# Optimization experiments

Measured on AMD Instinct MI355X. Metric: run time of the kernel, lower is better.

The kernel has to match this reference:

```python
import jax, jax.numpy as jnp
import numpy as np

S, B, I, H, L, O = 2048, 64, 64, 128, 2, 1


def _lstm_dir(xs, w_ih, w_hh, b, reverse):
    # xs: (S, B, in); w_ih: (4H, in); w_hh: (4H, H); b: (4H,) = b_ih + b_hh
    # PyTorch gate order: i, f, g, o
    gx = jnp.einsum('sbi,gi->sbg', xs, w_ih) + b  # precompute input gates once
    h0 = jnp.zeros((xs.shape[1], w_hh.shape[1]), xs.dtype)
    c0 = jnp.zeros_like(h0)

    def step(carry, g_t):
        h, c = carry
        g = g_t + h @ w_hh.T
        i, f, gg, o = jnp.split(g, 4, axis=-1)
        i = jax.nn.sigmoid(i)
        f = jax.nn.sigmoid(f)
        gg = jnp.tanh(gg)
        o = jax.nn.sigmoid(o)
        c = f * c + i * gg
        h = o * jnp.tanh(c)
        return (h, c), h

    _, hs = jax.lax.scan(step, (h0, c0), gx, reverse=reverse)
    return hs  # (S, B, H), time-aligned for both directions (PyTorch semantics)


def _bilstm(x, layers):
    out = x
    for (wif, whf, bf, wir, whr, br) in layers:
        hf = _lstm_dir(out, wif, whf, bf, reverse=False)
        hb = _lstm_dir(out, wir, whr, br, reverse=True)
        out = jnp.concatenate([hf, hb], axis=-1)  # (S, B, 2H)
    return out


def setup_inputs() -> dict:
    key = jax.random.key(0)
    ks = jax.random.split(key, 16)
    sc = 1.0 / np.sqrt(H)
    u = lambda k, shp: jax.random.uniform(k, shp, jnp.float32, -sc, sc)
    inp = {
        'x': jax.random.normal(ks[0], (S, B, I), jnp.float32),
        # layer 0 (input size I)
        'w_ih_f0': u(ks[1], (4 * H, I)), 'w_hh_f0': u(ks[2], (4 * H, H)), 'b_f0': u(ks[3], (4 * H,)),
        'w_ih_r0': u(ks[4], (4 * H, I)), 'w_hh_r0': u(ks[5], (4 * H, H)), 'b_r0': u(ks[6], (4 * H,)),
        # layer 1 (input size 2H)
        'w_ih_f1': u(ks[7], (4 * H, 2 * H)), 'w_hh_f1': u(ks[8], (4 * H, H)), 'b_f1': u(ks[9], (4 * H,)),
        'w_ih_r1': u(ks[10], (4 * H, 2 * H)), 'w_hh_r1': u(ks[11], (4 * H, H)), 'b_r1': u(ks[12], (4 * H,)),
        # final linear: (O, 2H), (O,)
        'w_out': u(ks[13], (O, 2 * H)), 'b_out': u(ks[14], (O,)),
    }
    return inp


def reference(x, w_ih_f0, w_hh_f0, b_f0, w_ih_r0, w_hh_r0, b_r0,
              w_ih_f1, w_hh_f1, b_f1, w_ih_r1, w_hh_r1, b_r1, w_out, b_out):
    layers = [
        (w_ih_f0, w_hh_f0, b_f0, w_ih_r0, w_hh_r0, b_r0),
        (w_ih_f1, w_hh_f1, b_f1, w_ih_r1, w_hh_r1, b_r1),
    ]
    h = _bilstm(x, layers)                      # (S, B, 2H)
    y = jnp.einsum('sbh,oh->sbo', h, w_out) + b_out  # linear over flattened (s*b, h)
    return y
```

## Files before the change

kernel.cpp:

```cpp
#include <hip/hip_runtime.h>
#include <hip/hip_bf16.h>

#define SEQ 2048
#define NB  64

typedef _Float16 f16x8 __attribute__((ext_vector_type(8)));
typedef _Float16 f16x4 __attribute__((ext_vector_type(4)));
typedef float    f32x4 __attribute__((ext_vector_type(4)));

__device__ __forceinline__ float fast_sigmoid(float x) {
    float e = __builtin_amdgcn_exp2f(-1.4426950408889634f * x);
    return __builtin_amdgcn_rcpf(1.f + e);
}
__device__ __forceinline__ float fast_tanh(float x) {
    float e = __builtin_amdgcn_exp2f(2.8853900817779268f * x);
    return fmaf(-2.f, __builtin_amdgcn_rcpf(1.f + e), 1.f);
}

__global__ __launch_bounds__(256) void split_f32(
    const float* __restrict__ s, _Float16* __restrict__ hi,
    _Float16* __restrict__ lo, int n)
{
    int i = blockIdx.x * 256 + threadIdx.x;
    if (i < n) {
        float v = s[i];
        _Float16 h = (_Float16)v;
        hi[i] = h;
        lo[i] = (_Float16)(v - (float)h);
    }
}

__global__ __launch_bounds__(256) void gemm0(
    const float* __restrict__ x,
    const _Float16* __restrict__ whi_f, const _Float16* __restrict__ wlo_f,
    const _Float16* __restrict__ whi_r, const _Float16* __restrict__ wlo_r,
    const float* __restrict__ bf_, const float* __restrict__ br_,
    float* __restrict__ gx, int tq0)
{
    const int lane = threadIdx.x & 63, wave = threadIdx.x >> 6;
    const int dir  = blockIdx.z;
    const _Float16* Whi = dir ? whi_r : whi_f;
    const _Float16* Wlo = dir ? wlo_r : wlo_f;
    const float* bias   = dir ? br_   : bf_;
    const int s   = blockIdx.y;
    const int t   = dir ? (SEQ - 1 - tq0 - s) : (tq0 + s);
    const int m0  = s * 64 + wave * 16;
    const int n0  = blockIdx.x * 64;
    const int col = lane & 15, kg = lane >> 4;

    f16x8 Bhi[4][2], Blo[4][2];
    #pragma unroll
    for (int nt = 0; nt < 4; ++nt)
        #pragma unroll
        for (int ks = 0; ks < 2; ++ks) {
            size_t idx = (size_t)(n0 + nt*16 + col) * 64 + ks*32 + kg*8;
            Bhi[nt][ks] = *(const f16x8*)(Whi + idx);
            Blo[nt][ks] = *(const f16x8*)(Wlo + idx);
        }
    f32x4 acc[4] = {{0,0,0,0},{0,0,0,0},{0,0,0,0},{0,0,0,0}};
    #pragma unroll
    for (int ks = 0; ks < 2; ++ks) {
        const float* ar = x + ((size_t)t*NB + wave*16 + col) * 64 + ks*32 + kg*8;
        float4 a0 = *(const float4*)ar;
        float4 a1 = *(const float4*)(ar + 4);
        f16x8 ahi, alo;
        float av[8] = {a0.x,a0.y,a0.z,a0.w,a1.x,a1.y,a1.z,a1.w};
        #pragma unroll
        for (int e = 0; e < 8; ++e) {
            _Float16 h = (_Float16)av[e];
            ahi[e] = h; alo[e] = (_Float16)(av[e] - (float)h);
        }
        #pragma unroll
        for (int nt = 0; nt < 4; ++nt) {
            acc[nt] = __builtin_amdgcn_mfma_f32_16x16x32_f16(ahi, Bhi[nt][ks], acc[nt], 0,0,0);
            acc[nt] = __builtin_amdgcn_mfma_f32_16x16x32_f16(ahi, Blo[nt][ks], acc[nt], 0,0,0);
            acc[nt] = __builtin_amdgcn_mfma_f32_16x16x32_f16(alo, Bhi[nt][ks], acc[nt], 0,0,0);
        }
    }
    #pragma unroll
    for (int nt = 0; nt < 4; ++nt) {
        const int n = n0 + nt*16 + col;
        const float bv = bias[n];
        #pragma unroll
        for (int r = 0; r < 4; ++r) {
            const int row = m0 + kg*4 + r;
            gx[(size_t)row * 1024 + dir*512 + n] = acc[nt][r] + bv;
        }
    }
}

template<int SPLIT_A>
__global__ __launch_bounds__(256) void gemm1(
    const _Float16* __restrict__ Ahi, const _Float16* __restrict__ Alo,
    const _Float16* __restrict__ whi_f, const _Float16* __restrict__ wlo_f,
    const _Float16* __restrict__ whi_r, const _Float16* __restrict__ wlo_r,
    const float* __restrict__ bf_, const float* __restrict__ br_,
    float* __restrict__ gx, int tq0)
{
    const int lane = threadIdx.x & 63, wave = threadIdx.x >> 6;
    const int dir  = blockIdx.z;
    const _Float16* Whi = dir ? whi_r : whi_f;
    const _Float16* Wlo = dir ? wlo_r : wlo_f;
    const float* bias   = dir ? br_   : bf_;
    const int wm = wave >> 1, wn = wave & 1;
    const int s  = blockIdx.y;
    const int t  = dir ? (SEQ - 1 - tq0 - s) : (tq0 + s);
    const int n0 = blockIdx.x * 64 + wn * 32;
    const int col = lane & 15, kg = lane >> 4;

    f16x8 Bhi[2][8], Blo[2][8];
    #pragma unroll
    for (int nt = 0; nt < 2; ++nt)
        #pragma unroll
        for (int ks = 0; ks < 8; ++ks) {
            size_t idx = (size_t)(n0 + nt*16 + col) * 256 + ks*32 + kg*8;
            Bhi[nt][ks] = *(const f16x8*)(Whi + idx);
            Blo[nt][ks] = *(const f16x8*)(Wlo + idx);
        }
    f32x4 acc[2][2] = {{{0,0,0,0},{0,0,0,0}},{{0,0,0,0},{0,0,0,0}}};
    #pragma unroll
    for (int ks = 0; ks < 8; ++ks) {
        #pragma unroll
        for (int mt = 0; mt < 2; ++mt) {
            const size_t arow = (size_t)t*NB + wm*32 + mt*16 + col;
            f16x8 ahi = *(const f16x8*)(Ahi + arow*256 + ks*32 + kg*8);
            f16x8 alo;
            if constexpr (SPLIT_A) alo = *(const f16x8*)(Alo + arow*256 + ks*32 + kg*8);
            #pragma unroll
            for (int nt = 0; nt < 2; ++nt) {
                acc[mt][nt] = __builtin_amdgcn_mfma_f32_16x16x32_f16(ahi, Bhi[nt][ks], acc[mt][nt], 0,0,0);
                acc[mt][nt] = __builtin_amdgcn_mfma_f32_16x16x32_f16(ahi, Blo[nt][ks], acc[mt][nt], 0,0,0);
                if constexpr (SPLIT_A)
                    acc[mt][nt] = __builtin_amdgcn_mfma_f32_16x16x32_f16(alo, Bhi[nt][ks], acc[mt][nt], 0,0,0);
            }
        }
    }
    #pragma unroll
    for (int mt = 0; mt < 2; ++mt)
        #pragma unroll
        for (int nt = 0; nt < 2; ++nt) {
            const int n = n0 + nt*16 + col;
            const float bv = bias[n];
            #pragma unroll
            for (int r = 0; r < 4; ++r) {
                const int row = s*64 + wm*32 + mt*16 + kg*4 + r;
                gx[(size_t)row * 1024 + dir*512 + n] = acc[mt][nt][r] + bv;
            }
        }
}

template<int OMODE>
__global__ __launch_bounds__(512) void lstm_rec(
    const float* __restrict__ gx,
    const float* __restrict__ Whf, const float* __restrict__ Whr,
    _Float16* __restrict__ o1, _Float16* __restrict__ o2,
    float* __restrict__ state, int tq0, int steps, int first)
{
    const int b   = blockIdx.x;
    const int dir = blockIdx.y;
    const float* Wh = dir ? Whr : Whf;
    const int j = threadIdx.x;

    float w[128];
    {
        const float4* wr = (const float4*)(Wh + (size_t)j * 128);
        #pragma unroll
        for (int q = 0; q < 32; ++q) {
            float4 v = wr[q];
            w[4*q+0]=v.x; w[4*q+1]=v.y; w[4*q+2]=v.z; w[4*q+3]=v.w;
        }
    }

    __shared__ float hsh[128];
    __shared__ float ash[512];
    float* st = state + ((size_t)dir*NB + b) * 256;
    if (j < 128) hsh[j] = first ? 0.f : st[j];
    float c = (j < 128) ? (first ? 0.f : st[128 + j]) : 0.f;
    const int type = j >> 7;
    const int k    = j & 127;
    __syncthreads();

    float gcur = gx[((size_t)b)*1024 + dir*512 + j];

    for (int step = 0; step < steps; ++step) {
        float gnext = 0.f;
        if (step + 1 < steps)
            gnext = gx[((size_t)(step+1)*NB + b)*1024 + dir*512 + j];
        float acc = gcur;
        #pragma unroll
        for (int q = 0; q < 32; ++q) {
            float4 h4 = *(const float4*)(hsh + 4*q);
            acc = fmaf(h4.x, w[4*q+0], acc);
            acc = fmaf(h4.y, w[4*q+1], acc);
            acc = fmaf(h4.z, w[4*q+2], acc);
            acc = fmaf(h4.w, w[4*q+3], acc);
        }
        float a = (type == 2) ? fast_tanh(acc) : fast_sigmoid(acc);
        ash[k*4 + type] = a;
        __syncthreads();
        if (j < 128) {
            float4 v = *(const float4*)(ash + j*4);
            c = fmaf(v.y, c, v.x * v.z);
            float h = v.w * fast_tanh(c);
            hsh[j] = h;
            const int t = dir ? (SEQ-1 - tq0 - step) : (tq0 + step);
            const size_t oi = ((size_t)t*NB + b)*256 + dir*128 + j;
            _Float16 hh = (_Float16)h;
            o1[oi] = hh;
            if constexpr (OMODE == 0) o2[oi] = (_Float16)(h - (float)hh);
        }
        __syncthreads();
        gcur = gnext;
    }
    if (j < 128) { st[j] = hsh[j]; st[128 + j] = c; }
}

__global__ __launch_bounds__(256) void final_lin(
    const _Float16* __restrict__ out1,
    const float* __restrict__ wout, const float* __restrict__ bout,
    float* __restrict__ y)
{
    const int lane = threadIdx.x & 63;
    const int wave = threadIdx.x >> 6;
    const int row  = blockIdx.x * 4 + wave;
    f16x4 u = *(const f16x4*)(out1 + (size_t)row*256 + lane*4);
    float4 wv = *(const float4*)(wout + lane*4);
    float s = (float)u[0]*wv.x + (float)u[1]*wv.y + (float)u[2]*wv.z + (float)u[3]*wv.w;
    #pragma unroll
    for (int off = 32; off > 0; off >>= 1) s += __shfl_down(s, off, 64);
    if (lane == 0) y[row] = s + bout[0];
}

extern "C" void kernel_launch(void* const* d_in, const int* in_sizes, int n_in,
                              void* d_out, int out_size, void* d_ws, size_t ws_size,
                              hipStream_t stream) {
    const float* x      = (const float*)d_in[0];
    const float* wih_f0 = (const float*)d_in[1];
    const float* whh_f0 = (const float*)d_in[2];
    const float* b_f0   = (const float*)d_in[3];
    const float* wih_r0 = (const float*)d_in[4];
    const float* whh_r0 = (const float*)d_in[5];
    const float* b_r0   = (const float*)d_in[6];
    const float* wih_f1 = (const float*)d_in[7];
    const float* whh_f1 = (const float*)d_in[8];
    const float* b_f1   = (const float*)d_in[9];
    const float* wih_r1 = (const float*)d_in[10];
    const float* whh_r1 = (const float*)d_in[11];
    const float* b_r1   = (const float*)d_in[12];
    const float* w_out  = (const float*)d_in[13];
    const float* b_out  = (const float*)d_in[14];

    const size_t w0N = 512*64, w1N = (size_t)512*256;
    const size_t w0B = w0N*2, w1B = w1N*2;
    const size_t stB = 128*256*4;
    const size_t hB  = (size_t)SEQ*NB*256*2;
    const size_t fixedB = 4*w0B + 4*w1B + stB;

    const int cand[7] = {2048, 1024, 512, 256, 128, 64, 32};
    int Tc = 0; int tierA = 1;
    for (int i = 0; i < 7 && !Tc; ++i)
        if (fixedB + 3*hB + (size_t)cand[i]*NB*1024*4 <= ws_size) Tc = cand[i];
    if (!Tc) {
        tierA = 0;
        for (int i = 0; i < 7 && !Tc; ++i)
            if (fixedB + 2*hB + (size_t)cand[i]*NB*1024*4 <= ws_size) Tc = cand[i];
        if (!Tc) Tc = 32;
    }
    const int nq = SEQ / Tc;

    char* p = (char*)d_ws;
    _Float16* whi0f = (_Float16*)p; p += w0B;
    _Float16* wlo0f = (_Float16*)p; p += w0B;
    _Float16* whi0r = (_Float16*)p; p += w0B;
    _Float16* wlo0r = (_Float16*)p; p += w0B;
    _Float16* whi1f = (_Float16*)p; p += w1B;
    _Float16* wlo1f = (_Float16*)p; p += w1B;
    _Float16* whi1r = (_Float16*)p; p += w1B;
    _Float16* wlo1r = (_Float16*)p; p += w1B;
    float*    state = (float*)p;    p += stB;
    _Float16* out1  = (_Float16*)p; p += hB;
    _Float16* h0hi  = (_Float16*)p; p += hB;
    _Float16* h0lo  = (_Float16*)p; if (tierA) p += hB;
    float*    gx    = (float*)p;

    split_f32<<<(int)((w0N+255)/256), 256, 0, stream>>>(wih_f0, whi0f, wlo0f, (int)w0N);
    split_f32<<<(int)((w0N+255)/256), 256, 0, stream>>>(wih_r0, whi0r, wlo0r, (int)w0N);
    split_f32<<<(int)((w1N+255)/256), 256, 0, stream>>>(wih_f1, whi1f, wlo1f, (int)w1N);
    split_f32<<<(int)((w1N+255)/256), 256, 0, stream>>>(wih_r1, whi1r, wlo1r, (int)w1N);

    for (int q = 0; q < nq; ++q) {
        gemm0<<<dim3(8, Tc, 2), 256, 0, stream>>>(x, whi0f, wlo0f, whi0r, wlo0r,
                                                  b_f0, b_r0, gx, q*Tc);
        if (tierA)
            lstm_rec<0><<<dim3(NB,2), 512, 0, stream>>>(gx, whh_f0, whh_r0, h0hi, h0lo,
                                                        state, q*Tc, Tc, q==0);
        else
            lstm_rec<1><<<dim3(NB,2), 512, 0, stream>>>(gx, whh_f0, whh_r0, h0hi, nullptr,
                                                        state, q*Tc, Tc, q==0);
    }
    for (int q = 0; q < nq; ++q) {
        if (tierA)
            gemm1<1><<<dim3(8, Tc, 2), 256, 0, stream>>>(h0hi, h0lo, whi1f, wlo1f, whi1r, wlo1r,
                                                         b_f1, b_r1, gx, q*Tc);
        else
            gemm1<0><<<dim3(8, Tc, 2), 256, 0, stream>>>(h0hi, h0hi, whi1f, wlo1f, whi1r, wlo1r,
                                                         b_f1, b_r1, gx, q*Tc);
        lstm_rec<1><<<dim3(NB,2), 512, 0, stream>>>(gx, whh_f1, whh_r1, out1, nullptr,
                                                    state, q*Tc, Tc, q==0);
    }
    final_lin<<<SEQ*NB/4, 256, 0, stream>>>(out1, w_out, b_out, (float*)d_out);
}
```

Before: 5.769 ms.

## Rewrite LSTM recurrence as MFMA over 8-batch groups with split-fp16 precision

The recurrent kernel moves from one block per batch element doing scalar FMA matvecs to one block per 8-batch group. That block runs the h·W_hh product with 16x16x32 fp16 MFMAs in a hi/lo split to keep fp32-level accuracy, and holds W_hh fragments in registers. The hidden state is double-buffered in swizzled shared memory so each step needs only one barrier instead of two. The gate GEMMs now write gx in an MFMA-fragment-native layout with vectorized f32x4 stores, so the recurrence can load its gates directly. In exchange only 16 blocks run, many MFMAs go to padded batch rows (only 8 of 16 rows are used), and each step does three MFMAs per tile.

```diff
diff --git a/kernel.cpp b/kernel.cpp
--- a/kernel.cpp
+++ b/kernel.cpp
@@ -29,6 +29,7 @@
         lo[i] = (_Float16)(v - (float)h);
     }
 }
+
 
 __global__ __launch_bounds__(256) void gemm0(
     const float* __restrict__ x,
@@ -44,7 +45,6 @@
     const float* bias   = dir ? br_   : bf_;
     const int s   = blockIdx.y;
     const int t   = dir ? (SEQ - 1 - tq0 - s) : (tq0 + s);
-    const int m0  = s * 64 + wave * 16;
     const int n0  = blockIdx.x * 64;
     const int col = lane & 15, kg = lane >> 4;
 
@@ -81,11 +81,9 @@
     for (int nt = 0; nt < 4; ++nt) {
         const int n = n0 + nt*16 + col;
         const float bv = bias[n];
-        #pragma unroll
-        for (int r = 0; r < 4; ++r) {
-            const int row = m0 + kg*4 + r;
-            gx[(size_t)row * 1024 + dir*512 + n] = acc[nt][r] + bv;
-        }
+        f32x4 v = {acc[nt][0]+bv, acc[nt][1]+bv, acc[nt][2]+bv, acc[nt][3]+bv};
+        size_t fi = (size_t)s*65536 + (dir*4 + wave)*8192 + (blockIdx.x*4 + nt)*256 + lane*4;
+        *(f32x4*)(gx + fi) = v;
     }
 }
 
@@ -141,78 +139,152 @@
         for (int nt = 0; nt < 2; ++nt) {
             const int n = n0 + nt*16 + col;
             const float bv = bias[n];
-            #pragma unroll
-            for (int r = 0; r < 4; ++r) {
-                const int row = s*64 + wm*32 + mt*16 + kg*4 + r;
-                gx[(size_t)row * 1024 + dir*512 + n] = acc[mt][nt][r] + bv;
-            }
+            f32x4 v = {acc[mt][nt][0]+bv, acc[mt][nt][1]+bv, acc[mt][nt][2]+bv, acc[mt][nt][3]+bv};
+            size_t fi = (size_t)s*65536 + (dir*4 + (wm*2+mt))*8192
+                      + (blockIdx.x*4 + wn*2 + nt)*256 + lane*4;
+            *(f32x4*)(gx + fi) = v;
         }
 }
 
 template<int OMODE>
-__global__ __launch_bounds__(512) void lstm_rec(
+__global__ __launch_bounds__(512, 2) void lstm_rec2(
     const float* __restrict__ gx,
     const float* __restrict__ Whf, const float* __restrict__ Whr,
     _Float16* __restrict__ o1, _Float16* __restrict__ o2,
-    float* __restrict__ state, int tq0, int steps, int first)
-{
-    const int b   = blockIdx.x;
+    float* __restrict__ state,
+    int tq0, int steps, int first)
+{
+    const int bg  = blockIdx.x;
     const int dir = blockIdx.y;
     const float* Wh = dir ? Whr : Whf;
-    const int j = threadIdx.x;
-
-    float w[128];
+    const int tid  = threadIdx.x;
+    const int w    = tid >> 6;
+    const int lane = tid & 63;
+    const int col  = lane & 15;
+    const int kg   = lane >> 4;
+    const int kidx = 16*w + col;
+
+    f16x8 Bhi[4][4], Blo[4][4];
+    #pragma unroll
+    for (int T = 0; T < 4; ++T) {
+        const float* wr = Wh + (size_t)((8*T + w)*16 + col) * 128;
+        #pragma unroll
+        for (int ks = 0; ks < 4; ++ks) {
+            const float* p4 = wr + ks*32 + kg*8;
+            float4 a0 = *(const float4*)p4, a1 = *(const float4*)(p4+4);
+            float av[8] = {a0.x,a0.y,a0.z,a0.w,a1.x,a1.y,a1.z,a1.w};
+            f16x8 hi, lo;
+            #pragma unroll
+            for (int e = 0; e < 8; ++e) {
+                _Float16 h = (_Float16)av[e];
+                hi[e] = h; lo[e] = (_Float16)(av[e] - (float)h);
+            }
+            Bhi[T][ks] = hi; Blo[T][ks] = lo;
+        }
+    }
+
+    __shared__ f16x8 Hhi[2][256];
+    __shared__ f16x8 Hlo[2][256];
+    for (int i = tid; i < 512; i += 512) { Hhi[0][0]; }
     {
-        const float4* wr = (const float4*)(Wh + (size_t)j * 128);
-        #pragma unroll
-        for (int q = 0; q < 32; ++q) {
-            float4 v = wr[q];
-            w[4*q+0]=v.x; w[4*q+1]=v.y; w[4*q+2]=v.z; w[4*q+3]=v.w;
-        }
-    }
-
-    __shared__ float hsh[128];
-    __shared__ float ash[512];
-    float* st = state + ((size_t)dir*NB + b) * 256;
-    if (j < 128) hsh[j] = first ? 0.f : st[j];
-    float c = (j < 128) ? (first ? 0.f : st[128 + j]) : 0.f;
-    const int type = j >> 7;
-    const int k    = j & 127;
+        f16x8 z = {};
+        if (tid < 512) { Hhi[tid>>8][tid&255] = z; Hlo[tid>>8][tid&255] = z; }
+    }
     __syncthreads();
 
-    float gcur = gx[((size_t)b)*1024 + dir*512 + j];
-
+    float cr[4] = {0,0,0,0};
+    float hr[4] = {0,0,0,0};
+    float* stbase = state + ((size_t)dir*8 + bg) * 2048;
+    if (!first && kg < 2) {
+        #pragma unroll
+        for (int r = 0; r < 4; ++r) {
+            const int m = kg*4 + r;
+            float hv = stbase[m*128 + kidx];
+            cr[r] = stbase[1024 + m*128 + kidx];
+            hr[r] = hv;
+            _Float16 hhi = (_Float16)hv;
+            _Float16 hlo = (_Float16)(hv - (float)hhi);
+            int el = (m*128 + kidx) ^ ((m&7)<<3);
+            ((_Float16*)Hhi[0])[el] = hhi;
+            ((_Float16*)Hlo[0])[el] = hlo;
+        }
+    }
+    __syncthreads();
+
+    const int lane2 = (kg + 2*(bg&1))*16 + col;
+    const int bgq   = bg >> 1;
+    const size_t gxo = (size_t)(dir*4 + bgq)*8192 + (size_t)lane2*4;
+
+    f32x4 gcur[4] = {{0,0,0,0},{0,0,0,0},{0,0,0,0},{0,0,0,0}};
+    if (kg < 2) {
+        #pragma unroll
+        for (int T = 0; T < 4; ++T)
+            gcur[T] = *(const f32x4*)(gx + gxo + (8*T + w)*256);
+    }
+
+    int p = 0;
     for (int step = 0; step < steps; ++step) {
-        float gnext = 0.f;
-        if (step + 1 < steps)
-            gnext = gx[((size_t)(step+1)*NB + b)*1024 + dir*512 + j];
-        float acc = gcur;
-        #pragma unroll
-        for (int q = 0; q < 32; ++q) {
-            float4 h4 = *(const float4*)(hsh + 4*q);
-            acc = fmaf(h4.x, w[4*q+0], acc);
-            acc = fmaf(h4.y, w[4*q+1], acc);
-            acc = fmaf(h4.z, w[4*q+2], acc);
-            acc = fmaf(h4.w, w[4*q+3], acc);
-        }
-        float a = (type == 2) ? fast_tanh(acc) : fast_sigmoid(acc);
-        ash[k*4 + type] = a;
+        f16x8 Ahi[4], Alo[4];
+        #pragma unroll
+        for (int ks = 0; ks < 4; ++ks) {
+            int idx = (col*16 + ks*4 + kg) ^ (col & 7);
+            Ahi[ks] = Hhi[p][idx];
+            Alo[ks] = Hlo[p][idx];
+        }
+        f32x4 gnx[4] = {{0,0,0,0},{0,0,0,0},{0,0,0,0},{0,0,0,0}};
+        if (step + 1 < steps && kg < 2) {
+            const size_t b = gxo + (size_t)(step+1)*65536;
+            #pragma unroll
+            for (int T = 0; T < 4; ++T)
+                gnx[T] = *(const f32x4*)(gx + b + (8*T + w)*256);
+        }
+        f32x4 acc[4];
+        #pragma unroll
+        for (int T = 0; T < 4; ++T) acc[T] = gcur[T];
+        #pragma unroll
+        for (int ks = 0; ks < 4; ++ks)
+            #pragma unroll
+            for (int T = 0; T < 4; ++T) {
+                acc[T] = __builtin_amdgcn_mfma_f32_16x16x32_f16(Ahi[ks], Bhi[T][ks], acc[T], 0,0,0);
+                acc[T] = __builtin_amdgcn_mfma_f32_16x16x32_f16(Alo[ks], Bhi[T][ks], acc[T], 0,0,0);
+                acc[T] = __builtin_amdgcn_mfma_f32_16x16x32_f16(Ahi[ks], Blo[T][ks], acc[T], 0,0,0);
+            }
+        if (kg < 2) {
+            const int t = dir ? (SEQ-1 - tq0 - step) : (tq0 + step);
+            #pragma unroll
+            for (int r = 0; r < 4; ++r) {
+                float iv = fast_sigmoid(acc[0][r]);
+                float fv = fast_sigmoid(acc[1][r]);
+                float gv = fast_tanh(acc[2][r]);
+                float ov = fast_sigmoid(acc[3][r]);
+                float cv = fmaf(fv, cr[r], iv * gv);
+                cr[r] = cv;
+                float hv = ov * fast_tanh(cv);
+                hr[r] = hv;
+                _Float16 hhi = (_Float16)hv;
+                _Float16 hlo = (_Float16)(hv - (float)hhi);
+                const int m = kg*4 + r;
+                int el = (m*128 + kidx) ^ ((m&7)<<3);
+                ((_Float16*)Hhi[p^1])[el] = hhi;
+                ((_Float16*)Hlo[p^1])[el] = hlo;
+                size_t oi = ((size_t)t*NB + (bg*8 + m))*256 + dir*128 + kidx;
+                o1[oi] = hhi;
+                if constexpr (OMODE == 0) o2[oi] = hlo;
+            }
+        }
         __syncthreads();
-        if (j < 128) {
-            float4 v = *(const float4*)(ash + j*4);
-            c = fmaf(v.y, c, v.x * v.z);
-            float h = v.w * fast_tanh(c);
-            hsh[j] = h;
-            const int t = dir ? (SEQ-1 - tq0 - step) : (tq0 + step);
-            const size_t oi = ((size_t)t*NB + b)*256 + dir*128 + j;
-            _Float16 hh = (_Float16)h;
-            o1[oi] = hh;
-            if constexpr (OMODE == 0) o2[oi] = (_Float16)(h - (float)hh);
-        }
-        __syncthreads();
-        gcur = gnext;
-    }
-    if (j < 128) { st[j] = hsh[j]; st[128 + j] = c; }
+        p ^= 1;
+        #pragma unroll
+        for (int T = 0; T < 4; ++T) gcur[T] = gnx[T];
+    }
+    if (kg < 2) {
+        #pragma unroll
+        for (int r = 0; r < 4; ++r) {
+            const int m = kg*4 + r;
+            stbase[m*128 + kidx] = hr[r];
+            stbase[1024 + m*128 + kidx] = cr[r];
+        }
+    }
 }
 
 __global__ __launch_bounds__(256) void final_lin(
@@ -252,7 +324,7 @@
 
     const size_t w0N = 512*64, w1N = (size_t)512*256;
     const size_t w0B = w0N*2, w1B = w1N*2;
-    const size_t stB = 128*256*4;
+    const size_t stB = 2*8*2048*4;
     const size_t hB  = (size_t)SEQ*NB*256*2;
     const size_t fixedB = 4*w0B + 4*w1B + stB;
 
@@ -292,10 +364,10 @@
         gemm0<<<dim3(8, Tc, 2), 256, 0, stream>>>(x, whi0f, wlo0f, whi0r, wlo0r,
                                                   b_f0, b_r0, gx, q*Tc);
         if (tierA)
-            lstm_rec<0><<<dim3(NB,2), 512, 0, stream>>>(gx, whh_f0, whh_r0, h0hi, h0lo,
+            lstm_rec2<0><<<dim3(8,2), 512, 0, stream>>>(gx, whh_f0, whh_r0, h0hi, h0lo,
                                                         state, q*Tc, Tc, q==0);
         else
-            lstm_rec<1><<<dim3(NB,2), 512, 0, stream>>>(gx, whh_f0, whh_r0, h0hi, nullptr,
+            lstm_rec2<1><<<dim3(8,2), 512, 0, stream>>>(gx, whh_f0, whh_r0, h0hi, nullptr,
                                                         state, q*Tc, Tc, q==0);
     }
     for (int q = 0; q < nq; ++q) {
@@ -305,7 +377,7 @@
         else
             gemm1<0><<<dim3(8, Tc, 2), 256, 0, stream>>>(h0hi, h0hi, whi1f, wlo1f, whi1r, wlo1r,
                                                          b_f1, b_r1, gx, q*Tc);
-        lstm_rec<1><<<dim3(NB,2), 512, 0, stream>>>(gx, whh_f1, whh_r1, out1, nullptr,
+        lstm_rec2<1><<<dim3(8,2), 512, 0, stream>>>(gx, whh_f1, whh_r1, out1, nullptr,
                                                     state, q*Tc, Tc, q==0);
     }
     final_lin<<<SEQ*NB/4, 256, 0, stream>>>(out1, w_out, b_out, (float*)d_out);
```

New measurement: 7.962 ms. +38.0%, slower.
